# Kernel tuning notes

Measured on AMD Instinct MI355X. Metric: run time of the kernel, lower is better.

Reference implementation:

```python
import jax, jax.numpy as jnp
import numpy as np

EMBED = 384
HEAD = 64


def setup_inputs() -> dict:
    key = jax.random.key(0)
    kx, kq, kk, kv = jax.random.split(key, 4)
    B, T = 4, 4096
    x = jax.random.normal(kx, (B, T, EMBED), dtype=jnp.float32)
    # torch Linear(384, 64, bias=False): weight (64, 384), y = x @ W.T.
    # Store pre-transposed as (EMBED, HEAD) so y = x @ W.
    s = 1.0 / np.sqrt(EMBED)  # kaiming-uniform-ish scale
    Wq = jax.random.uniform(kq, (EMBED, HEAD), jnp.float32, -s, s)
    Wk = jax.random.uniform(kk, (EMBED, HEAD), jnp.float32, -s, s)
    Wv = jax.random.uniform(kv, (EMBED, HEAD), jnp.float32, -s, s)
    return {"x": x, "Wq": Wq, "Wk": Wk, "Wv": Wv}


def reference(x, Wq, Wk, Wv):
    # q, k, v: [B, T, H]
    q = x @ Wq
    k = x @ Wk
    v = x @ Wv
    scale = k.shape[-1] ** (-0.5)
    scores = jnp.einsum("bth,bsh->bts", q, k) * scale  # [B, T, T]
    # Faithful to the original: tril, then mask anything equal to 0 with -inf
    # (this also masks exact zeros inside the causal region).
    tril = jnp.tril(scores)
    masked = jnp.where(tril == 0, -jnp.inf, tril)
    attn = jax.nn.softmax(masked, axis=-1)
    out = jnp.einsum("bts,bsh->bth", attn, v)  # [B, T, H]
    return out
```

## Files before the change

### kernel.cpp

```cpp
#include <hip/hip_runtime.h>
#include <hip/hip_bf16.h>
#include <stdint.h>


#define EMBED 384
#define HEAD  64
#define NB    4
#define NT    4096
#define NROWS (NB * NT)

#define SCALE_Q 0.18033688011112042f

typedef short bf16x8 __attribute__((ext_vector_type(8)));
typedef float f32x4  __attribute__((ext_vector_type(4)));

__device__ __forceinline__ unsigned short bfround(float f) {
    union { float f; unsigned u; } v; v.f = f;
    return (unsigned short)((v.u + 0x8000u) >> 16);
}
__device__ __forceinline__ unsigned packbf(float lo, float hi) {
    union { float f; unsigned u; } a, b; a.f = lo; b.f = hi;
    return ((a.u + 0x8000u) >> 16) | ((b.u + 0x8000u) & 0xFFFF0000u);
}

__global__ __launch_bounds__(256)
void wprep_kernel(const float* __restrict__ Wq,
                  const float* __restrict__ Wk,
                  const float* __restrict__ Wv,
                  unsigned short* __restrict__ Wt)
{
    int idx = blockIdx.x * 256 + threadIdx.x;
    int k = idx / 192;
    int n = idx - k * 192;
    int sel = n >> 6, nc = n & 63;
    const float* wp = (sel == 0) ? Wq : ((sel == 1) ? Wk : Wv);
    Wt[n * EMBED + k] = bfround(wp[(size_t)k * HEAD + nc]);
}

__global__ __launch_bounds__(256)
void proj_kernel(const float* __restrict__ x,
                 const unsigned short* __restrict__ Wt,
                 unsigned short* __restrict__ Qo,
                 unsigned short* __restrict__ Ko,
                 unsigned short* __restrict__ Vto)
{
    __shared__ __attribute__((aligned(16))) unsigned short ws[96][200];
    __shared__ __attribute__((aligned(16))) unsigned short xs[64][200];
    unsigned short (*vbuf)[72] = (unsigned short (*)[72])&xs[0][0];

    const int t    = threadIdx.x;
    const int w    = t >> 6;
    const int lane = t & 63;
    const int quad = lane >> 4;
    const int l16  = lane & 15;
    const int half = blockIdx.x & 1;
    const int r0   = (blockIdx.x >> 1) * 64;
    const int colbase = half * 96;

    f32x4 acc[6];
#pragma unroll
    for (int i = 0; i < 6; ++i) acc[i] = (f32x4){0.f, 0.f, 0.f, 0.f};

#pragma unroll
    for (int ph = 0; ph < 2; ++ph) {
        if (ph) __syncthreads();
        const int k0 = ph * 192;
#pragma unroll
        for (int i = 0; i < 9; ++i) {
            int idx = t + i * 256;
            int row = idx / 24, c = idx - row * 24;
            *(uint4*)&ws[row][c * 8] =
                *(const uint4*)(Wt + (size_t)(colbase + row) * EMBED + k0 + c * 8);
        }
#pragma unroll
        for (int i = 0; i < 12; ++i) {
            int idx = t + i * 256;
            int row = idx / 48, c4 = idx - row * 48;
            const float4 v = *(const float4*)(x + (size_t)(r0 + row) * EMBED + k0 + c4 * 4);
            uint2 pw; pw.x = packbf(v.x, v.y); pw.y = packbf(v.z, v.w);
            *(uint2*)&xs[row][c4 * 4] = pw;
        }
        __syncthreads();
#pragma unroll
        for (int step = 0; step < 6; ++step) {
            bf16x8 a = *(const bf16x8*)&xs[w * 16 + l16][step * 32 + quad * 8];
#pragma unroll
            for (int ng = 0; ng < 6; ++ng) {
                bf16x8 b = *(const bf16x8*)&ws[ng * 16 + l16][step * 32 + quad * 8];
                acc[ng] = __builtin_amdgcn_mfma_f32_16x16x32_bf16(a, b, acc[ng], 0, 0, 0);
            }
        }
    }
    __syncthreads();

#pragma unroll
    for (int ng = 0; ng < 6; ++ng) {
        int cg = colbase + ng * 16 + l16;
#pragma unroll
        for (int r = 0; r < 4; ++r) {
            int row = r0 + w * 16 + quad * 4 + r;
            float vv = acc[ng][r];
            if (cg < 64) {
                Qo[(size_t)row * HEAD + cg] = bfround(vv * SCALE_Q);
            } else if (cg < 128) {
                Ko[(size_t)row * HEAD + (cg - 64)] = bfround(vv);
            } else {
                vbuf[cg - 128][w * 16 + quad * 4 + r] = bfround(vv);
            }
        }
    }
    __syncthreads();
    if (half == 1) {
        const int batch = r0 >> 12;
        const int s0 = r0 & (NT - 1);
#pragma unroll
        for (int i = 0; i < 2; ++i) {
            int idx = t + i * 256;
            int d = idx >> 3, c = idx & 7;
            *(uint4*)(Vto + ((size_t)(batch * HEAD + d)) * NT + s0 + c * 8) =
                *(const uint4*)&vbuf[d][c * 8];
        }
    }
}

__global__ __launch_bounds__(256)
void attn_kernel(const unsigned short* __restrict__ Qi,
                 const unsigned short* __restrict__ Ki,
                 const unsigned short* __restrict__ Vti,
                 float* __restrict__ opart,
                 float* __restrict__ lpart)
{
    __shared__ __attribute__((aligned(16))) unsigned short Kt[64][64];
    __shared__ __attribute__((aligned(16))) unsigned short Vs[64][64];
    __shared__ __attribute__((aligned(16))) unsigned short Ps[4][16][72];

    const int t    = threadIdx.x;
    const int w    = t >> 6;
    const int lane = t & 63;
    const int quad = lane >> 4;
    const int l16  = lane & 15;

    const int u = blockIdx.x;
    int m, sp, batch;
    if (u < 256) { m = 63 - (u >> 2); sp = 0; batch = u & 3; }
    else         { int v = u - 256; m = v >> 2; sp = 1; batch = v & 3; }
    const int ntiles = (m >= sp) ? (((m - sp) >> 1) + 1) : 0;
    const int q0 = m * 64 + w * 16;

    const unsigned short* Kbg = Ki  + (size_t)batch * NT * HEAD;
    const unsigned short* Vbg = Vti + (size_t)batch * HEAD * NT;

    bf16x8 bq0, bq1;
    {
        const unsigned short* qp = Qi + (size_t)(batch * NT + q0 + l16) * HEAD + quad * 8;
        bq0 = *(const bf16x8*)(qp);
        bq1 = *(const bf16x8*)(qp + 32);
    }

    f32x4 o[4];
#pragma unroll
    for (int i = 0; i < 4; ++i) o[i] = (f32x4){0.f, 0.f, 0.f, 0.f};
    float rs = 0.f;

    const int srow0 = t >> 3, sc = t & 7;
    const int srow1 = (t + 256) >> 3;
    const int scc0 = sc ^ (srow0 & 7);
    const int scc1 = sc ^ (srow1 & 7);

    for (int j = 0; j < ntiles; ++j) {
        const int kt = sp + 2 * j;
        uint4 kr0 = *(const uint4*)(Kbg + (size_t)(kt * 64 + srow0) * HEAD + sc * 8);
        uint4 kr1 = *(const uint4*)(Kbg + (size_t)(kt * 64 + srow1) * HEAD + sc * 8);
        uint4 vr0 = *(const uint4*)(Vbg + (size_t)srow0 * NT + kt * 64 + sc * 8);
        uint4 vr1 = *(const uint4*)(Vbg + (size_t)srow1 * NT + kt * 64 + sc * 8);
        __syncthreads();
        *(uint4*)&Kt[srow0][scc0 * 8] = kr0;
        *(uint4*)&Kt[srow1][scc1 * 8] = kr1;
        *(uint4*)&Vs[srow0][scc0 * 8] = vr0;
        *(uint4*)&Vs[srow1][scc1 * 8] = vr1;
        __syncthreads();

        const int sw = l16 & 7;
        const bool diag = (kt == m);
#pragma unroll
        for (int ts = 0; ts < 4; ++ts) {
            bf16x8 ak0 = *(const bf16x8*)&Kt[ts * 16 + l16][(quad ^ sw) * 8];
            bf16x8 ak1 = *(const bf16x8*)&Kt[ts * 16 + l16][((4 + quad) ^ sw) * 8];
            f32x4 z = (f32x4){0.f, 0.f, 0.f, 0.f};
            z = __builtin_amdgcn_mfma_f32_16x16x32_bf16(ak0, bq0, z, 0, 0, 0);
            z = __builtin_amdgcn_mfma_f32_16x16x32_bf16(ak1, bq1, z, 0, 0, 0);
            float p[4];
#pragma unroll
            for (int r = 0; r < 4; ++r) {
                float pv = __builtin_amdgcn_exp2f(z[r]);
                if (diag) {
                    int sg = kt * 64 + ts * 16 + quad * 4 + r;
                    pv = (sg > q0 + l16) ? 0.f : pv;
                }
                p[r] = pv;
            }
            rs += (p[0] + p[1]) + (p[2] + p[3]);
            uint2 pw; pw.x = packbf(p[0], p[1]); pw.y = packbf(p[2], p[3]);
            *(uint2*)&Ps[w][l16][ts * 16 + quad * 4] = pw;
        }
        bf16x8 ap0 = *(const bf16x8*)&Ps[w][l16][quad * 8];
        bf16x8 ap1 = *(const bf16x8*)&Ps[w][l16][32 + quad * 8];
#pragma unroll
        for (int nd = 0; nd < 4; ++nd) {
            bf16x8 av0 = *(const bf16x8*)&Vs[nd * 16 + l16][(quad ^ sw) * 8];
            bf16x8 av1 = *(const bf16x8*)&Vs[nd * 16 + l16][((4 + quad) ^ sw) * 8];
            o[nd] = __builtin_amdgcn_mfma_f32_16x16x32_bf16(ap0, av0, o[nd], 0, 0, 0);
            o[nd] = __builtin_amdgcn_mfma_f32_16x16x32_bf16(ap1, av1, o[nd], 0, 0, 0);
        }
    }

    rs += __shfl_xor(rs, 16, 64);
    rs += __shfl_xor(rs, 32, 64);
    if (quad == 0)
        lpart[(size_t)sp * NROWS + batch * NT + q0 + l16] = rs;
    float* ob = opart + (size_t)sp * NROWS * HEAD;
#pragma unroll
    for (int r = 0; r < 4; ++r) {
        size_t off = (size_t)(batch * NT + q0 + quad * 4 + r) * HEAD;
#pragma unroll
        for (int nd = 0; nd < 4; ++nd)
            ob[off + nd * 16 + l16] = o[nd][r];
    }
}

__global__ __launch_bounds__(256)
void combine_kernel(const float* __restrict__ opart,
                    const float* __restrict__ lpart,
                    float* __restrict__ out)
{
    int gid = blockIdx.x * 256 + threadIdx.x;
    int row = gid >> 4;
    int d4  = (gid & 15) * 4;
    f32x4 a = *(const f32x4*)(opart + (size_t)row * HEAD + d4);
    f32x4 b = *(const f32x4*)(opart + (size_t)NROWS * HEAD + (size_t)row * HEAD + d4);
    float inv = 1.0f / (lpart[row] + lpart[NROWS + row]);
    f32x4 res = (a + b);
    res[0] *= inv; res[1] *= inv; res[2] *= inv; res[3] *= inv;
    *(f32x4*)(out + (size_t)row * HEAD + d4) = res;
}

extern "C" void kernel_launch(void* const* d_in, const int* in_sizes, int n_in,
                              void* d_out, int out_size, void* d_ws, size_t ws_size,
                              hipStream_t stream)
{
    const float* x  = (const float*)d_in[0];
    const float* Wq = (const float*)d_in[1];
    const float* Wk = (const float*)d_in[2];
    const float* Wv = (const float*)d_in[3];
    float* out = (float*)d_out;

    unsigned short* Qw  = (unsigned short*)d_ws;
    unsigned short* Kw  = Qw + (size_t)NROWS * HEAD;
    unsigned short* Vtw = Kw + (size_t)NROWS * HEAD;
    unsigned short* Wtw = Vtw + (size_t)NROWS * HEAD;
    float* opart = (float*)(Wtw + (size_t)192 * EMBED);
    float* lpart = opart + (size_t)2 * NROWS * HEAD;

    wprep_kernel<<<(192 * EMBED) / 256, 256, 0, stream>>>(Wq, Wk, Wv, Wtw);
    proj_kernel<<<512, 256, 0, stream>>>(x, Wtw, Qw, Kw, Vtw);
    attn_kernel<<<512, 256, 0, stream>>>(Qw, Kw, Vtw, opart, lpart);
    combine_kernel<<<NROWS * 16 / 256, 256, 0, stream>>>(opart, lpart, out);
}
```

Baseline: 128.1 us.

## Split attention KV four ways, double-buffer K/V tiles, permlane P transpose

Raises the key-split factor from 2 to 4 so the attention launch grows from 512 to 1024 blocks, and widens the combine kernel to sum four partials. The K/V tiles are now double-buffered in LDS, with the next tile's global loads issued before compute so each iteration needs one barrier instead of two. The P tile is rearranged into the MFMA A-operand layout in registers with v_permlane swap instructions instead of a round trip through LDS. The cost is twice the partial-output traffic and work in combine, more LDS per block, and a launch-bounds occupancy hint that may constrain registers.

Result: faster. 106.4 us (-16.9%).

```diff
diff --git a/kernel.cpp b/kernel.cpp
--- a/kernel.cpp
+++ b/kernel.cpp
@@ -8,6 +8,7 @@
 #define NB    4
 #define NT    4096
 #define NROWS (NB * NT)
+#define NSPLIT 4
 
 #define SCALE_Q 0.18033688011112042f
 
@@ -21,6 +22,13 @@
 __device__ __forceinline__ unsigned packbf(float lo, float hi) {
     union { float f; unsigned u; } a, b; a.f = lo; b.f = hi;
     return ((a.u + 0x8000u) >> 16) | ((b.u + 0x8000u) & 0xFFFF0000u);
+}
+
+__device__ __forceinline__ void pl_swap32(unsigned& a, unsigned& b) {
+    asm("v_permlane32_swap_b32 %0, %1" : "+v"(a), "+v"(b));
+}
+__device__ __forceinline__ void pl_swap16(unsigned& a, unsigned& b) {
+    asm("v_permlane16_swap_b32 %0, %1" : "+v"(a), "+v"(b));
 }
 
 __global__ __launch_bounds__(256)
@@ -123,16 +131,15 @@
     }
 }
 
-__global__ __launch_bounds__(256)
+__global__ __launch_bounds__(256, 4)
 void attn_kernel(const unsigned short* __restrict__ Qi,
                  const unsigned short* __restrict__ Ki,
                  const unsigned short* __restrict__ Vti,
                  float* __restrict__ opart,
                  float* __restrict__ lpart)
 {
-    __shared__ __attribute__((aligned(16))) unsigned short Kt[64][64];
-    __shared__ __attribute__((aligned(16))) unsigned short Vs[64][64];
-    __shared__ __attribute__((aligned(16))) unsigned short Ps[4][16][72];
+    __shared__ __attribute__((aligned(16))) unsigned short Kt[2][64][64];
+    __shared__ __attribute__((aligned(16))) unsigned short Vs[2][64][64];
 
     const int t    = threadIdx.x;
     const int w    = t >> 6;
@@ -141,10 +148,11 @@
     const int l16  = lane & 15;
 
     const int u = blockIdx.x;
-    int m, sp, batch;
-    if (u < 256) { m = 63 - (u >> 2); sp = 0; batch = u & 3; }
-    else         { int v = u - 256; m = v >> 2; sp = 1; batch = v & 3; }
-    const int ntiles = (m >= sp) ? (((m - sp) >> 1) + 1) : 0;
+    const int g = u >> 4;
+    const int m = (g < 32) ? (63 - g) : (g - 32);
+    const int sp = (u >> 2) & 3;
+    const int batch = u & 3;
+    const int ntiles = (m >= sp) ? (((m - sp) >> 2) + 1) : 0;
     const int q0 = m * 64 + w * 16;
 
     const unsigned short* Kbg = Ki  + (size_t)batch * NT * HEAD;
@@ -166,26 +174,40 @@
     const int srow1 = (t + 256) >> 3;
     const int scc0 = sc ^ (srow0 & 7);
     const int scc1 = sc ^ (srow1 & 7);
-
+    const int sw = l16 & 7;
+
+    uint4 kr0, kr1, vr0, vr1;
+    if (ntiles > 0) {
+        const int kt = sp;
+        kr0 = *(const uint4*)(Kbg + (size_t)(kt * 64 + srow0) * HEAD + sc * 8);
+        kr1 = *(const uint4*)(Kbg + (size_t)(kt * 64 + srow1) * HEAD + sc * 8);
+        vr0 = *(const uint4*)(Vbg + (size_t)srow0 * NT + kt * 64 + sc * 8);
+        vr1 = *(const uint4*)(Vbg + (size_t)srow1 * NT + kt * 64 + sc * 8);
+    }
+
+    int cur = 0;
     for (int j = 0; j < ntiles; ++j) {
-        const int kt = sp + 2 * j;
-        uint4 kr0 = *(const uint4*)(Kbg + (size_t)(kt * 64 + srow0) * HEAD + sc * 8);
-        uint4 kr1 = *(const uint4*)(Kbg + (size_t)(kt * 64 + srow1) * HEAD + sc * 8);
-        uint4 vr0 = *(const uint4*)(Vbg + (size_t)srow0 * NT + kt * 64 + sc * 8);
-        uint4 vr1 = *(const uint4*)(Vbg + (size_t)srow1 * NT + kt * 64 + sc * 8);
+        const int kt = sp + 4 * j;
+        *(uint4*)&Kt[cur][srow0][scc0 * 8] = kr0;
+        *(uint4*)&Kt[cur][srow1][scc1 * 8] = kr1;
+        *(uint4*)&Vs[cur][srow0][scc0 * 8] = vr0;
+        *(uint4*)&Vs[cur][srow1][scc1 * 8] = vr1;
         __syncthreads();
-        *(uint4*)&Kt[srow0][scc0 * 8] = kr0;
-        *(uint4*)&Kt[srow1][scc1 * 8] = kr1;
-        *(uint4*)&Vs[srow0][scc0 * 8] = vr0;
-        *(uint4*)&Vs[srow1][scc1 * 8] = vr1;
-        __syncthreads();
-
-        const int sw = l16 & 7;
+
+        if (j + 1 < ntiles) {
+            const int ktn = kt + 4;
+            kr0 = *(const uint4*)(Kbg + (size_t)(ktn * 64 + srow0) * HEAD + sc * 8);
+            kr1 = *(const uint4*)(Kbg + (size_t)(ktn * 64 + srow1) * HEAD + sc * 8);
+            vr0 = *(const uint4*)(Vbg + (size_t)srow0 * NT + ktn * 64 + sc * 8);
+            vr1 = *(const uint4*)(Vbg + (size_t)srow1 * NT + ktn * 64 + sc * 8);
+        }
+
         const bool diag = (kt == m);
+        uint2 pw[4];
 #pragma unroll
         for (int ts = 0; ts < 4; ++ts) {
-            bf16x8 ak0 = *(const bf16x8*)&Kt[ts * 16 + l16][(quad ^ sw) * 8];
-            bf16x8 ak1 = *(const bf16x8*)&Kt[ts * 16 + l16][((4 + quad) ^ sw) * 8];
+            bf16x8 ak0 = *(const bf16x8*)&Kt[cur][ts * 16 + l16][(quad ^ sw) * 8];
+            bf16x8 ak1 = *(const bf16x8*)&Kt[cur][ts * 16 + l16][((4 + quad) ^ sw) * 8];
             f32x4 z = (f32x4){0.f, 0.f, 0.f, 0.f};
             z = __builtin_amdgcn_mfma_f32_16x16x32_bf16(ak0, bq0, z, 0, 0, 0);
             z = __builtin_amdgcn_mfma_f32_16x16x32_bf16(ak1, bq1, z, 0, 0, 0);
@@ -200,18 +222,30 @@
                 p[r] = pv;
             }
             rs += (p[0] + p[1]) + (p[2] + p[3]);
-            uint2 pw; pw.x = packbf(p[0], p[1]); pw.y = packbf(p[2], p[3]);
-            *(uint2*)&Ps[w][l16][ts * 16 + quad * 4] = pw;
-        }
-        bf16x8 ap0 = *(const bf16x8*)&Ps[w][l16][quad * 8];
-        bf16x8 ap1 = *(const bf16x8*)&Ps[w][l16][32 + quad * 8];
+            pw[ts].x = packbf(p[0], p[1]);
+            pw[ts].y = packbf(p[2], p[3]);
+        }
+
+        unsigned a0 = pw[0].x, c0 = pw[0].y, b0 = pw[1].x, d0 = pw[1].y;
+        pl_swap32(a0, b0); pl_swap32(c0, d0);
+        pl_swap16(a0, b0); pl_swap16(c0, d0);
+        unsigned a1 = pw[2].x, c1 = pw[2].y, b1 = pw[3].x, d1 = pw[3].y;
+        pl_swap32(a1, b1); pl_swap32(c1, d1);
+        pl_swap16(a1, b1); pl_swap16(c1, d1);
+        union { unsigned u[4]; bf16x8 v; } ua0, ua1;
+        ua0.u[0] = a0; ua0.u[1] = c0; ua0.u[2] = b0; ua0.u[3] = d0;
+        ua1.u[0] = a1; ua1.u[1] = c1; ua1.u[2] = b1; ua1.u[3] = d1;
+        const bf16x8 ap0 = ua0.v;
+        const bf16x8 ap1 = ua1.v;
+
 #pragma unroll
         for (int nd = 0; nd < 4; ++nd) {
-            bf16x8 av0 = *(const bf16x8*)&Vs[nd * 16 + l16][(quad ^ sw) * 8];
-            bf16x8 av1 = *(const bf16x8*)&Vs[nd * 16 + l16][((4 + quad) ^ sw) * 8];
+            bf16x8 av0 = *(const bf16x8*)&Vs[cur][nd * 16 + l16][(quad ^ sw) * 8];
+            bf16x8 av1 = *(const bf16x8*)&Vs[cur][nd * 16 + l16][((4 + quad) ^ sw) * 8];
             o[nd] = __builtin_amdgcn_mfma_f32_16x16x32_bf16(ap0, av0, o[nd], 0, 0, 0);
             o[nd] = __builtin_amdgcn_mfma_f32_16x16x32_bf16(ap1, av1, o[nd], 0, 0, 0);
         }
+        cur ^= 1;
     }
 
     rs += __shfl_xor(rs, 16, 64);
@@ -236,10 +270,15 @@
     int gid = blockIdx.x * 256 + threadIdx.x;
     int row = gid >> 4;
     int d4  = (gid & 15) * 4;
-    f32x4 a = *(const f32x4*)(opart + (size_t)row * HEAD + d4);
-    f32x4 b = *(const f32x4*)(opart + (size_t)NROWS * HEAD + (size_t)row * HEAD + d4);
-    float inv = 1.0f / (lpart[row] + lpart[NROWS + row]);
-    f32x4 res = (a + b);
+    const size_t st = (size_t)NROWS * HEAD;
+    const float* p0 = opart + (size_t)row * HEAD + d4;
+    f32x4 a = *(const f32x4*)(p0);
+    f32x4 b = *(const f32x4*)(p0 + st);
+    f32x4 c = *(const f32x4*)(p0 + 2 * st);
+    f32x4 d = *(const f32x4*)(p0 + 3 * st);
+    float inv = 1.0f / (lpart[row] + lpart[NROWS + row] +
+                        lpart[2 * NROWS + row] + lpart[3 * NROWS + row]);
+    f32x4 res = (a + b) + (c + d);
     res[0] *= inv; res[1] *= inv; res[2] *= inv; res[3] *= inv;
     *(f32x4*)(out + (size_t)row * HEAD + d4) = res;
 }
@@ -259,10 +298,10 @@
     unsigned short* Vtw = Kw + (size_t)NROWS * HEAD;
     unsigned short* Wtw = Vtw + (size_t)NROWS * HEAD;
     float* opart = (float*)(Wtw + (size_t)192 * EMBED);
-    float* lpart = opart + (size_t)2 * NROWS * HEAD;
+    float* lpart = opart + (size_t)NSPLIT * NROWS * HEAD;
 
     wprep_kernel<<<(192 * EMBED) / 256, 256, 0, stream>>>(Wq, Wk, Wv, Wtw);
     proj_kernel<<<512, 256, 0, stream>>>(x, Wtw, Qw, Kw, Vtw);
-    attn_kernel<<<512, 256, 0, stream>>>(Qw, Kw, Vtw, opart, lpart);
+    attn_kernel<<<1024, 256, 0, stream>>>(Qw, Kw, Vtw, opart, lpart);
     combine_kernel<<<NROWS * 16 / 256, 256, 0, stream>>>(opart, lpart, out);
 }
```
